# Kernel optimization log

Hardware: AMD Instinct MI355X
Metric: run time of the kernel (lower is better)

The kernel has to match this reference:

```python
import jax, jax.numpy as jnp
import numpy as np

CLIP = 1.3   # FastSign STE clamp range (FracBNN-style)
EPS = 1e-5   # BatchNorm eps

@jax.custom_vjp
def fast_sign(x):
    # forward: sign(x); backward: straight-through grad of clamp(x, -1.3, 1.3)
    return jnp.sign(x)

def _fs_fwd(x):
    return jnp.sign(x), x

def _fs_bwd(res, g):
    return (g * (jnp.abs(res) <= CLIP).astype(g.dtype),)

fast_sign.defvjp(_fs_fwd, _fs_bwd)

def conv(x, w, pad):
    return jax.lax.conv_general_dilated(
        x, w, window_strides=(1, 1), padding=[(pad, pad), (pad, pad)],
        dimension_numbers=('NCHW', 'OIHW', 'NCHW'))

def bn(x, gamma, beta, mean, var):
    # eval-mode BatchNorm2d folded into a single scale/shift
    inv = gamma * jax.lax.rsqrt(var + EPS)
    return x * inv[None, :, None, None] + (beta - mean * inv)[None, :, None, None]

def setup_inputs() -> dict:
    key = jax.random.key(0)
    ks = jax.random.split(key, 11)
    C = 32
    x = jax.random.normal(ks[0], (32, C, 160, 160), jnp.float32)
    w3 = jax.random.normal(ks[1], (C, C, 3, 3), jnp.float32) * 0.1
    g3 = jax.random.uniform(ks[2], (C,), jnp.float32, 0.5, 1.5)
    b3 = jax.random.normal(ks[3], (C,), jnp.float32) * 0.1
    m3 = jax.random.normal(ks[4], (C,), jnp.float32) * 0.1
    v3 = jax.random.uniform(ks[5], (C,), jnp.float32, 0.5, 1.5)
    w1 = jax.random.normal(ks[6], (C, C, 1, 1), jnp.float32) * 0.1
    g1 = jax.random.uniform(ks[7], (C,), jnp.float32, 0.5, 1.5)
    b1 = jax.random.normal(ks[8], (C,), jnp.float32) * 0.1
    m1 = jax.random.normal(ks[9], (C,), jnp.float32) * 0.1
    v1 = jax.random.uniform(ks[10], (C,), jnp.float32, 0.5, 1.5)
    return {"x": x, "w3": w3, "g3": g3, "b3": b3, "m3": m3, "v3": v3,
            "w1": w1, "g1": g1, "b1": b1, "m1": m1, "v1": v1}

def reference(x, w3, g3, b3, m3, v3, w1, g1, b1, m1, v1):
    # block 1: binarize -> 3x3 binary conv -> BN -> residual
    y = bn(conv(fast_sign(x), fast_sign(w3), 1), g3, b3, m3, v3) + x
    # block 2: binarize -> 1x1 binary conv -> BN -> residual
    z = bn(conv(fast_sign(y), fast_sign(w1), 0), g1, b1, m1, v1) + y
    return z
```

## Files before the change

### kernel.cpp

```cpp
#include <hip/hip_runtime.h>
#include <stdint.h>

#define C   32
#define H   160
#define W   160
#define NB  32
#define HW  (H * W)
#define CHW (C * HW)
#define NPIX (NB * HW)
#define XBOFF 448


__global__ void pack_params(const float* __restrict__ w3,
                            const float* __restrict__ g3, const float* __restrict__ b3,
                            const float* __restrict__ m3, const float* __restrict__ v3,
                            const float* __restrict__ w1,
                            const float* __restrict__ g1, const float* __restrict__ b1,
                            const float* __restrict__ m1, const float* __restrict__ v1,
                            uint32_t* __restrict__ wsu) {
    int t = threadIdx.x;
    if (t < 288) {
        int oc = t / 9, tap = t % 9;
        uint32_t bits = 0;
#pragma unroll
        for (int ic = 0; ic < 32; ++ic)
            bits |= (w3[oc * 288 + ic * 9 + tap] < 0.0f) ? (1u << ic) : 0u;
        wsu[t] = bits;
    } else if (t < 320) {
        int oc = t - 288;
        uint32_t bits = 0;
#pragma unroll
        for (int ic = 0; ic < 32; ++ic)
            bits |= (w1[oc * 32 + ic] < 0.0f) ? (1u << ic) : 0u;
        wsu[288 + oc] = bits;
        float* f = (float*)wsu;
        float inv3 = g3[oc] * rsqrtf(v3[oc] + 1e-5f);
        f[320 + oc] = inv3;
        f[352 + oc] = b3[oc] - m3[oc] * inv3;
        float inv1 = g1[oc] * rsqrtf(v1[oc] + 1e-5f);
        f[384 + oc] = inv1;
        f[416 + oc] = b1[oc] - m1[oc] * inv1;
    }
}

__global__ __launch_bounds__(256) void pack_x(const float* __restrict__ x,
                                              uint32_t* __restrict__ xbits) {
    int i = blockIdx.x * blockDim.x + threadIdx.x;
    if (i >= NPIX / 4) return;
    int p = i * 4;
    int n = p / HW;
    int r = p % HW;
    const float* xp = x + n * CHW + r;
    uint32_t b0 = 0, b1 = 0, b2 = 0, b3 = 0;
#pragma unroll
    for (int c = 0; c < 32; ++c) {
        float4 v = *reinterpret_cast<const float4*>(xp + c * HW);
        b0 |= (v.x < 0.0f) ? (1u << c) : 0u;
        b1 |= (v.y < 0.0f) ? (1u << c) : 0u;
        b2 |= (v.z < 0.0f) ? (1u << c) : 0u;
        b3 |= (v.w < 0.0f) ? (1u << c) : 0u;
    }
    *reinterpret_cast<uint4*>(xbits + p) = make_uint4(b0, b1, b2, b3);
}

__global__ __launch_bounds__(256) void fused_main(const float* __restrict__ x,
                                                  const uint32_t* __restrict__ wsu,
                                                  float* __restrict__ out) {
    const float* wf = (const float*)wsu;
    int pi = blockIdx.x * blockDim.x + threadIdx.x;
    int p0  = pi * 2;
    int n   = p0 / HW;
    int rem = p0 % HW;
    int h   = rem / W;
    int w   = rem % W;

    const uint32_t* xbn = wsu + XBOFF + n * HW;

    int hm1 = (h > 0) ? h - 1 : 0;
    int hp1 = (h < H - 1) ? h + 1 : H - 1;
    int wm1 = (w > 0) ? w - 1 : 0;
    int wp2 = (w < W - 2) ? w + 2 : W - 1;

    uint32_t nb[3][4];
    {
        const uint32_t* r0 = xbn + hm1 * W;
        const uint32_t* r1 = xbn + h   * W;
        const uint32_t* r2 = xbn + hp1 * W;
        nb[0][0] = r0[wm1]; nb[0][1] = r0[w]; nb[0][2] = r0[w + 1]; nb[0][3] = r0[wp2];
        nb[1][0] = r1[wm1]; nb[1][1] = r1[w]; nb[1][2] = r1[w + 1]; nb[1][3] = r1[wp2];
        nb[2][0] = r2[wm1]; nb[2][1] = r2[w]; nb[2][2] = r2[w + 1]; nb[2][3] = r2[wp2];
    }

    const float* xrow = x + n * CHW + h * W + w;
    float y0[32], y1[32];

#pragma unroll
    for (int oc = 0; oc < 32; ++oc) {
        int s0 = 0, s1 = 0;
#pragma unroll
        for (int r = 0; r < 3; ++r) {
#pragma unroll
            for (int c = 0; c < 3; ++c) {
                uint32_t wv = wsu[oc * 9 + r * 3 + c];
                s0 += __popc(nb[r][c] ^ wv);
                s1 += __popc(nb[r][c + 1] ^ wv);
            }
        }
        float sc = wf[320 + oc], sh = wf[352 + oc];
        float2 xv = *reinterpret_cast<const float2*>(xrow + oc * HW);
        y0[oc] = fmaf((float)(288 - 2 * s0), sc, sh) + xv.x;
        y1[oc] = fmaf((float)(288 - 2 * s1), sc, sh) + xv.y;
    }

    uint32_t yb0 = 0, yb1 = 0;
#pragma unroll
    for (int oc = 0; oc < 32; ++oc) {
        yb0 |= (y0[oc] < 0.0f) ? (1u << oc) : 0u;
        yb1 |= (y1[oc] < 0.0f) ? (1u << oc) : 0u;
    }
    float* orow = out + n * CHW + h * W + w;
#pragma unroll
    for (int oc = 0; oc < 32; ++oc) {
        float sc = wf[384 + oc], sh = wf[416 + oc];
        int c0 = 32 - 2 * __popc(yb0 ^ wsu[288 + oc]);
        int c1 = 32 - 2 * __popc(yb1 ^ wsu[288 + oc]);
        float2 zv;
        zv.x = fmaf((float)c0, sc, sh) + y0[oc];
        zv.y = fmaf((float)c1, sc, sh) + y1[oc];
        *reinterpret_cast<float2*>(orow + oc * HW) = zv;
    }
}

__global__ __launch_bounds__(256) void border_fix(const float* __restrict__ x,
                                                  const uint32_t* __restrict__ wsu,
                                                  float* __restrict__ out) {
    const float* wf = (const float*)wsu;
    int t = blockIdx.x * blockDim.x + threadIdx.x;
    if (t >= NB * 636) return;
    int n = t / 636, idx = t % 636;
    int h, w;
    if (idx < 160)      { h = 0;         w = idx; }
    else if (idx < 320) { h = H - 1;     w = idx - 160; }
    else if (idx < 478) { h = idx - 319; w = 0; }
    else                { h = idx - 477; w = W - 1; }

    const uint32_t* xbn = wsu + XBOFF + n * HW;
    uint32_t nb[3][3];
    int m[3][3];
#pragma unroll
    for (int r = 0; r < 3; ++r) {
        int hh = h + r - 1;
        bool rok = (hh >= 0) && (hh < H);
#pragma unroll
        for (int c = 0; c < 3; ++c) {
            int ww = w + c - 1;
            bool ok = rok && (ww >= 0) && (ww < W);
            m[r][c]  = ok ? -1 : 0;
            nb[r][c] = ok ? xbn[hh * W + ww] : 0u;
        }
    }

    const float* xp = x + n * CHW + h * W + w;
    float y[32];
    uint32_t yb = 0;
#pragma unroll
    for (int oc = 0; oc < 32; ++oc) {
        int s = 0;
#pragma unroll
        for (int r = 0; r < 3; ++r) {
#pragma unroll
            for (int c = 0; c < 3; ++c) {
                uint32_t wv = wsu[oc * 9 + r * 3 + c];
                s += (32 - 2 * __popc(nb[r][c] ^ wv)) & m[r][c];
            }
        }
        float sc = wf[320 + oc], sh = wf[352 + oc];
        y[oc] = fmaf((float)s, sc, sh) + xp[oc * HW];
        yb |= (y[oc] < 0.0f) ? (1u << oc) : 0u;
    }
    float* op = out + n * CHW + h * W + w;
#pragma unroll
    for (int oc = 0; oc < 32; ++oc) {
        float sc = wf[384 + oc], sh = wf[416 + oc];
        int cc = 32 - 2 * __popc(yb ^ wsu[288 + oc]);
        op[oc * HW] = fmaf((float)cc, sc, sh) + y[oc];
    }
}

extern "C" void kernel_launch(void* const* d_in, const int* in_sizes, int n_in,
                              void* d_out, int out_size, void* d_ws, size_t ws_size,
                              hipStream_t stream) {
    const float* x  = (const float*)d_in[0];
    const float* w3 = (const float*)d_in[1];
    const float* g3 = (const float*)d_in[2];
    const float* b3 = (const float*)d_in[3];
    const float* m3 = (const float*)d_in[4];
    const float* v3 = (const float*)d_in[5];
    const float* w1 = (const float*)d_in[6];
    const float* g1 = (const float*)d_in[7];
    const float* b1 = (const float*)d_in[8];
    const float* m1 = (const float*)d_in[9];
    const float* v1 = (const float*)d_in[10];
    float* out = (float*)d_out;
    uint32_t* wsu = (uint32_t*)d_ws;

    pack_params<<<1, 320, 0, stream>>>(w3, g3, b3, m3, v3, w1, g1, b1, m1, v1, wsu);
    pack_x<<<NPIX / 4 / 256, 256, 0, stream>>>(x, wsu + XBOFF);
    fused_main<<<NPIX / 2 / 256, 256, 0, stream>>>(x, wsu, out);
    border_fix<<<(NB * 636 + 255) / 256, 256, 0, stream>>>(x, wsu, out);
}
```

Baseline: 84.43 us.

## Fuse sign-packing of x into tiled main kernel via shared-memory halo

Drops the separate pack_x kernel and its global bit-plane buffer. Each block now handles an 8-row tile of one image: it packs sign bits for the tile plus a one-row halo into shared memory, synchronizes, then runs the binary 3x3 and 1x1 convolutions from LDS. This saves a kernel launch and a global write/read of the packed bits, at the cost of re-reading 2 halo rows of x per tile and a block-wide barrier. The border kernel now packs its neighbour bits straight from x with strided scalar loads.

```diff
diff --git a/kernel.cpp b/kernel.cpp
--- a/kernel.cpp
+++ b/kernel.cpp
@@ -8,7 +8,9 @@
 #define HW  (H * W)
 #define CHW (C * HW)
 #define NPIX (NB * HW)
-#define XBOFF 448
+#define TH  8
+#define NTILES (H / TH)
+#define NTHR (TH * W / 2)
 
 
 __global__ void pack_params(const float* __restrict__ w3,
@@ -43,67 +45,64 @@
     }
 }
 
-__global__ __launch_bounds__(256) void pack_x(const float* __restrict__ x,
-                                              uint32_t* __restrict__ xbits) {
-    int i = blockIdx.x * blockDim.x + threadIdx.x;
-    if (i >= NPIX / 4) return;
-    int p = i * 4;
-    int n = p / HW;
-    int r = p % HW;
-    const float* xp = x + n * CHW + r;
-    uint32_t b0 = 0, b1 = 0, b2 = 0, b3 = 0;
-#pragma unroll
-    for (int c = 0; c < 32; ++c) {
-        float4 v = *reinterpret_cast<const float4*>(xp + c * HW);
-        b0 |= (v.x < 0.0f) ? (1u << c) : 0u;
-        b1 |= (v.y < 0.0f) ? (1u << c) : 0u;
-        b2 |= (v.z < 0.0f) ? (1u << c) : 0u;
-        b3 |= (v.w < 0.0f) ? (1u << c) : 0u;
-    }
-    *reinterpret_cast<uint4*>(xbits + p) = make_uint4(b0, b1, b2, b3);
-}
-
-__global__ __launch_bounds__(256) void fused_main(const float* __restrict__ x,
-                                                  const uint32_t* __restrict__ wsu,
-                                                  float* __restrict__ out) {
+__global__ __launch_bounds__(NTHR) void fused_tile(const float* __restrict__ x,
+                                                   const uint32_t* __restrict__ wsu,
+                                                   float* __restrict__ out) {
+    __shared__ uint32_t sbits[(TH + 2) * W];
     const float* wf = (const float*)wsu;
-    int pi = blockIdx.x * blockDim.x + threadIdx.x;
-    int p0  = pi * 2;
-    int n   = p0 / HW;
-    int rem = p0 % HW;
-    int h   = rem / W;
-    int w   = rem % W;
-
-    const uint32_t* xbn = wsu + XBOFF + n * HW;
-
-    int hm1 = (h > 0) ? h - 1 : 0;
-    int hp1 = (h < H - 1) ? h + 1 : H - 1;
+    int bid  = blockIdx.x;
+    int n    = bid / NTILES;
+    int tile = bid % NTILES;
+    int h0   = tile * TH;
+    const float* xn = x + n * CHW;
+    int t = threadIdx.x;
+
+    if (t < (TH + 2) * W / 4) {
+        int prow = t / (W / 4);
+        int qcol = (t % (W / 4)) * 4;
+        int hh = h0 - 1 + prow;
+        hh = (hh < 0) ? 0 : (hh > H - 1 ? H - 1 : hh);
+        const float* xp = xn + hh * W + qcol;
+        uint32_t b0 = 0, b1 = 0, b2 = 0, b3 = 0;
+#pragma unroll
+        for (int c = 0; c < 32; ++c) {
+            float4 v = *reinterpret_cast<const float4*>(xp + c * HW);
+            b0 |= (v.x < 0.0f) ? (1u << c) : 0u;
+            b1 |= (v.y < 0.0f) ? (1u << c) : 0u;
+            b2 |= (v.z < 0.0f) ? (1u << c) : 0u;
+            b3 |= (v.w < 0.0f) ? (1u << c) : 0u;
+        }
+        *reinterpret_cast<uint4*>(&sbits[t * 4]) = make_uint4(b0, b1, b2, b3);
+    }
+    __syncthreads();
+
+    int r = t / (W / 2);
+    int w = (t % (W / 2)) * 2;
+    int h = h0 + r;
+
     int wm1 = (w > 0) ? w - 1 : 0;
     int wp2 = (w < W - 2) ? w + 2 : W - 1;
 
     uint32_t nb[3][4];
-    {
-        const uint32_t* r0 = xbn + hm1 * W;
-        const uint32_t* r1 = xbn + h   * W;
-        const uint32_t* r2 = xbn + hp1 * W;
-        nb[0][0] = r0[wm1]; nb[0][1] = r0[w]; nb[0][2] = r0[w + 1]; nb[0][3] = r0[wp2];
-        nb[1][0] = r1[wm1]; nb[1][1] = r1[w]; nb[1][2] = r1[w + 1]; nb[1][3] = r1[wp2];
-        nb[2][0] = r2[wm1]; nb[2][1] = r2[w]; nb[2][2] = r2[w + 1]; nb[2][3] = r2[wp2];
-    }
-
-    const float* xrow = x + n * CHW + h * W + w;
+#pragma unroll
+    for (int dr = 0; dr < 3; ++dr) {
+        const uint32_t* rp = &sbits[(r + dr) * W];
+        nb[dr][0] = rp[wm1]; nb[dr][1] = rp[w];
+        nb[dr][2] = rp[w + 1]; nb[dr][3] = rp[wp2];
+    }
+
+    const float* xrow = xn + h * W + w;
     float y0[32], y1[32];
-
 #pragma unroll
     for (int oc = 0; oc < 32; ++oc) {
         int s0 = 0, s1 = 0;
 #pragma unroll
-        for (int r = 0; r < 3; ++r) {
+        for (int dr = 0; dr < 3; ++dr) {
 #pragma unroll
             for (int c = 0; c < 3; ++c) {
-                uint32_t wv = wsu[oc * 9 + r * 3 + c];
-                s0 += __popc(nb[r][c] ^ wv);
-                s1 += __popc(nb[r][c + 1] ^ wv);
+                uint32_t wv = wsu[oc * 9 + dr * 3 + c];
+                s0 += __popc(nb[dr][c] ^ wv);
+                s1 += __popc(nb[dr][c + 1] ^ wv);
             }
         }
         float sc = wf[320 + oc], sh = wf[352 + oc];
@@ -144,7 +143,7 @@
     else if (idx < 478) { h = idx - 319; w = 0; }
     else                { h = idx - 477; w = W - 1; }
 
-    const uint32_t* xbn = wsu + XBOFF + n * HW;
+    const float* xn = x + n * CHW;
     uint32_t nb[3][3];
     int m[3][3];
 #pragma unroll
@@ -155,12 +154,19 @@
         for (int c = 0; c < 3; ++c) {
             int ww = w + c - 1;
             bool ok = rok && (ww >= 0) && (ww < W);
-            m[r][c]  = ok ? -1 : 0;
-            nb[r][c] = ok ? xbn[hh * W + ww] : 0u;
-        }
-    }
-
-    const float* xp = x + n * CHW + h * W + w;
+            m[r][c] = ok ? -1 : 0;
+            uint32_t bits = 0;
+            if (ok) {
+                const float* xp = xn + hh * W + ww;
+#pragma unroll
+                for (int ch = 0; ch < 32; ++ch)
+                    bits |= (xp[ch * HW] < 0.0f) ? (1u << ch) : 0u;
+            }
+            nb[r][c] = bits;
+        }
+    }
+
+    const float* xp = xn + h * W + w;
     float y[32];
     uint32_t yb = 0;
 #pragma unroll
@@ -205,7 +211,6 @@
     uint32_t* wsu = (uint32_t*)d_ws;
 
     pack_params<<<1, 320, 0, stream>>>(w3, g3, b3, m3, v3, w1, g1, b1, m1, v1, wsu);
-    pack_x<<<NPIX / 4 / 256, 256, 0, stream>>>(x, wsu + XBOFF);
-    fused_main<<<NPIX / 2 / 256, 256, 0, stream>>>(x, wsu, out);
+    fused_tile<<<NB * NTILES, NTHR, 0, stream>>>(x, wsu, out);
     border_fix<<<(NB * 636 + 255) / 256, 256, 0, stream>>>(x, wsu, out);
 }
```

Result: slower. 163.8 us (+94.0%).
